# Performance work log

Hardware: AMD Instinct MI355X
Metric: run time of the kernel (lower is better)

## Reference

```python
import jax, jax.numpy as jnp
import numpy as np

B, S, D_IN = 16, 512, 768
HID, OUT = 64, 12
NEG = 1e12


def setup_inputs() -> dict:
    key = jax.random.key(0)
    k1, k2, k3 = jax.random.split(key, 3)
    x = jax.random.normal(k1, (B, S, D_IN), dtype=jnp.float32)
    mask = jnp.ones((B, S), dtype=jnp.float32)
    W = jax.random.normal(k2, (D_IN, HID * OUT * 2), dtype=jnp.float32) * 0.02
    b = jax.random.normal(k3, (HID * OUT * 2,), dtype=jnp.float32) * 0.02
    return {"x": x, "mask": mask, "W": W, "b": b}


def reference(x, mask, W, b):
    Bb, Ss, _ = x.shape
    h, out = HID, OUT
    # QKV-style projection, split into `out` heads of 2h each
    proj = (x @ W + b).reshape(Bb, Ss, out, 2 * h)  # [b, s, out, 2h]
    qw, kw = proj[..., :h], proj[..., h:]           # [b, s, out, h]

    # Sinusoidal position embedding (merge='zero'): interleaved sin/cos
    pos_ids = jnp.arange(Ss, dtype=x.dtype)
    inv_freq = jnp.power(10000.0, -2.0 * jnp.arange(h // 2, dtype=x.dtype) / h)
    ang = pos_ids[:, None] * inv_freq               # [s, h/2]
    sin, cos = jnp.sin(ang), jnp.cos(ang)
    # torch: pos[..., None, 1::2].repeat(1,1,1,2) -> TILED (not interleaved)
    cos_pos = jnp.concatenate([cos, cos], axis=-1)[None, :, None, :]  # [1, s, 1, h]
    sin_pos = jnp.concatenate([sin, sin], axis=-1)[None, :, None, :]

    def rope(w):
        # stack([-w_odd, w_even], -1).reshape -> interleaved rotation partner
        w2 = jnp.stack([-w[..., 1::2], w[..., ::2]], axis=-1).reshape(w.shape)
        return w * cos_pos + w2 * sin_pos

    qw = rope(qw)
    kw = rope(kw)

    logits = jnp.einsum('bmhd,bnhd->bhmn', qw, kw)  # [b, out, s, s]

    pad = mask[:, None, None, :]                    # broadcast over [b, out, s, s]
    logits = logits * pad - (1.0 - pad) * NEG

    tril = jnp.tril(jnp.ones((Ss, Ss), dtype=logits.dtype), -1)
    logits = logits - tril * NEG

    return logits / (h ** 0.5)
```

## Files before the change

### kernel.cpp

```cpp
#include <hip/hip_runtime.h>
#include <stdint.h>

#define DIN   768
#define NPROJ 1536
#define SEQ   512
#define NHEAD 12
#define NBATCH 16
#define NEGV  1000000000000.0f

typedef short bf16x8 __attribute__((ext_vector_type(8)));
typedef float f32x4  __attribute__((ext_vector_type(4)));
typedef unsigned short u16x8 __attribute__((ext_vector_type(8)));

__device__ __forceinline__ unsigned short f2bf(float f) {
    union { float f; unsigned int u; } v; v.f = f;
    return (unsigned short)((v.u + 0x7FFFu + ((v.u >> 16) & 1u)) >> 16);
}
__device__ __forceinline__ float bf2f(unsigned short u) {
    union { unsigned int u; float f; } v; v.u = ((unsigned int)u) << 16;
    return v.f;
}

__device__ __forceinline__ void gl_lds16(const unsigned short* g, unsigned short* l) {
    __builtin_amdgcn_global_load_lds(
        (const __attribute__((address_space(1))) unsigned int*)(uintptr_t)g,
        (__attribute__((address_space(3))) unsigned int*)(uintptr_t)l,
        16, 0, 0);
}

__device__ __forceinline__ void stage128x64(const unsigned short* __restrict__ g,
                                            int gstride, unsigned short* lds,
                                            int w, int lane) {
#pragma unroll
    for (int t = 0; t < 4; t++) {
        int lr = w * 32 + t * 8 + (lane >> 3);
        int c16 = (lane & 7) ^ (lr & 7);
        gl_lds16(g + (size_t)lr * gstride + c16 * 8,
                 lds + (w * 32 + t * 8) * 64);
    }
}
__device__ __forceinline__ int swz(int row, int cg) {
    return row * 64 + ((cg ^ (row & 7)) << 3);
}

__global__ __launch_bounds__(256) void k_prep(const float* __restrict__ X,
                                              unsigned short* __restrict__ Xb,
                                              const float* __restrict__ W,
                                              unsigned short* __restrict__ Wt,
                                              float* __restrict__ trig) {
    __shared__ unsigned short T[64][72];
    const int bid = blockIdx.x, tid = threadIdx.x;
    if (bid < 288) {
        int n0 = (bid % 24) * 64, k0 = (bid / 24) * 64;
#pragma unroll
        for (int it = 0; it < 4; it++) {
            int c = tid + it * 256;
            int kl = c >> 4, nl = (c & 15) * 4;
            float4 v = *(const float4*)&W[(size_t)(k0 + kl) * NPROJ + n0 + nl];
            T[nl + 0][kl] = f2bf(v.x);
            T[nl + 1][kl] = f2bf(v.y);
            T[nl + 2][kl] = f2bf(v.z);
            T[nl + 3][kl] = f2bf(v.w);
        }
        __syncthreads();
#pragma unroll
        for (int it = 0; it < 2; it++) {
            int c = tid + it * 256;
            int nl = c >> 3, kb = (c & 7) * 8;
            *(int4*)&Wt[(size_t)(n0 + nl) * DIN + k0 + kb] = *(int4*)&T[nl][kb];
        }
        return;
    }
    if (bid < 352) {
        int gi = (bid - 288) * 256 + tid;
        int ss = gi >> 5, j = gi & 31;
        const float C = 0.41524101186092034f;
        float cs, sn;
        sincosf((float)ss * exp2f(-(float)j * C), &sn, &cs);
        trig[2 * gi]     = cs;
        trig[2 * gi + 1] = sn;
        return;
    }
    int i = ((bid - 352) * 256 + tid) * 4;
    float4 v = *(const float4*)&X[i];
    short4 s;
    s.x = (short)f2bf(v.x); s.y = (short)f2bf(v.y);
    s.z = (short)f2bf(v.z); s.w = (short)f2bf(v.w);
    *(short4*)&Xb[i] = s;
}

template <bool PRE>
__global__ __launch_bounds__(256) void k_gemm(const float* __restrict__ X,
                                              const unsigned short* __restrict__ Xb,
                                              const unsigned short* __restrict__ Wt,
                                              const float* __restrict__ bias,
                                              const float* __restrict__ trig,
                                              unsigned short* __restrict__ P) {
    __shared__ unsigned short smem[17408];
    unsigned short* sA = smem;
    unsigned short* sB = smem + 8192;
    const int tid = threadIdx.x;
    const int m0 = blockIdx.y * 128, n0 = blockIdx.x * 128;
    const int lane = tid & 63, w = tid >> 6;
    const int q = lane >> 4, r = lane & 15;
    const int wm = w >> 1, wn = w & 1;
    f32x4 acc[4][4];
#pragma unroll
    for (int i = 0; i < 4; i++)
#pragma unroll
        for (int j = 0; j < 4; j++) acc[i][j] = (f32x4){0.f, 0.f, 0.f, 0.f};

    const unsigned short* Ag = Xb + (size_t)m0 * DIN;
    const unsigned short* Bg = Wt + (size_t)n0 * DIN;

    for (int k0 = 0; k0 < DIN; k0 += 64) {
        __syncthreads();
        if (PRE) {
            stage128x64(Ag + k0, DIN, sA, w, lane);
        } else {
#pragma unroll
            for (int it = 0; it < 4; it++) {
                int c = tid + it * 256;
                int row = c >> 3, c16 = c & 7;
                const float* xp = &X[(size_t)(m0 + row) * DIN + k0 + c16 * 8];
                float4 v0 = *(const float4*)xp;
                float4 v1 = *(const float4*)(xp + 4);
                u16x8 sv;
                sv[0] = f2bf(v0.x); sv[1] = f2bf(v0.y);
                sv[2] = f2bf(v0.z); sv[3] = f2bf(v0.w);
                sv[4] = f2bf(v1.x); sv[5] = f2bf(v1.y);
                sv[6] = f2bf(v1.z); sv[7] = f2bf(v1.w);
                *(u16x8*)&sA[swz(row, c16)] = sv;
            }
        }
        stage128x64(Bg + k0, DIN, sB, w, lane);
        __syncthreads();
#pragma unroll
        for (int kk = 0; kk < 64; kk += 32) {
            const int cg = (kk >> 3) + q;
            bf16x8 af[4], bfr[4];
#pragma unroll
            for (int t = 0; t < 4; t++)
                af[t] = *(const bf16x8*)&sA[swz(wm * 64 + t * 16 + r, cg)];
#pragma unroll
            for (int t = 0; t < 4; t++)
                bfr[t] = *(const bf16x8*)&sB[swz(wn * 64 + t * 16 + r, cg)];
#pragma unroll
            for (int tm = 0; tm < 4; tm++)
#pragma unroll
                for (int tn = 0; tn < 4; tn++)
                    acc[tm][tn] = __builtin_amdgcn_mfma_f32_16x16x32_bf16(
                        af[tm], bfr[tn], acc[tm][tn], 0, 0, 0);
        }
    }
    float bb[4];
#pragma unroll
    for (int tn = 0; tn < 4; tn++) bb[tn] = bias[n0 + wn * 64 + tn * 16 + r];
    __syncthreads();
    unsigned short* sT = smem;
#pragma unroll
    for (int tm = 0; tm < 4; tm++) {
        int rowb = wm * 64 + tm * 16 + q * 4;
#pragma unroll
        for (int tn = 0; tn < 4; tn++) {
            int col = wn * 64 + tn * 16 + r;
#pragma unroll
            for (int i = 0; i < 4; i++)
                sT[(rowb + i) * 136 + col] = f2bf(acc[tm][tn][i] + bb[tn]);
        }
    }
    __syncthreads();
#pragma unroll
    for (int it = 0; it < 8; it++) {
        int c = tid + it * 256;
        int row = c >> 4, colb = (c & 15) * 8;
        int m = m0 + row;
        int s = m & (SEQ - 1);
        int base = colb & 31;
        union { int4 v; unsigned short u[8]; } pk;
        pk.v = *(int4*)&sT[row * 136 + colb];
        float wv[8];
#pragma unroll
        for (int j = 0; j < 8; j++) wv[j] = bf2f(pk.u[j]);
        const float* tp = &trig[2 * (s * 32 + base)];
#pragma unroll
        for (int p = 0; p < 4; p++) {
            float4 tt = *(const float4*)&tp[4 * p];
            float oe = wv[2 * p] * tt.x - wv[2 * p + 1] * tt.y;
            float oo = wv[2 * p + 1] * tt.z + wv[2 * p] * tt.w;
            pk.u[2 * p]     = f2bf(oe);
            pk.u[2 * p + 1] = f2bf(oo);
        }
        *(int4*)&P[(size_t)m * NPROJ + n0 + colb] = pk.v;
    }
}

__global__ __launch_bounds__(256) void k_attn(const unsigned short* __restrict__ P,
                                              const float* __restrict__ mask,
                                              float* __restrict__ out) {
    __shared__ unsigned short sQ[8192], sK[8192];
    __shared__ float sbuf[32 * 132];
    const int tid = threadIdx.x;
    const int b = blockIdx.z, h = blockIdx.y, mt = blockIdx.x;
    const int lane = tid & 63, w = tid >> 6;
    const int q = lane >> 4, r = lane & 15;
    const int wm = w >> 1, wn = w & 1;
    const size_t obase = ((size_t)((b * NHEAD + h) * SEQ)) * SEQ;

    const unsigned short* Qg = P + (size_t)(b * SEQ + mt * 128) * NPROJ + h * 128;
    stage128x64(Qg, NPROJ, sQ, w, lane);

    bf16x8 aq[2][4];
    bool qload = false;
    for (int nt = 0; nt < 4; nt++) {
        const int ncol0 = nt * 128;
        if (nt < mt) {
#pragma unroll
            for (int it = 0; it < 16; it++) {
                int c = tid + it * 256;
                int rl = c >> 5, cb = (c & 31) * 4;
                int m = mt * 128 + rl, n = ncol0 + cb;
                f32x4 mk = *(const f32x4*)&mask[b * SEQ + n];
                f32x4 o;
#pragma unroll
                for (int j = 0; j < 4; j++)
                    o[j] = (-(1.f - mk[j]) * NEGV - NEGV) * 0.125f;
                __builtin_nontemporal_store(o, (f32x4*)&out[obase + (size_t)m * SEQ + n]);
            }
            continue;
        }
        __syncthreads();
        const unsigned short* Kg =
            P + (size_t)(b * SEQ + nt * 128) * NPROJ + h * 128 + 64;
        stage128x64(Kg, NPROJ, sK, w, lane);
        __syncthreads();
        if (!qload) {
            qload = true;
#pragma unroll
            for (int x2 = 0; x2 < 2; x2++) {
                int cg = x2 * 4 + q;
#pragma unroll
                for (int t = 0; t < 4; t++)
                    aq[x2][t] = *(const bf16x8*)&sQ[swz(wm * 64 + t * 16 + r, cg)];
            }
        }
        f32x4 acc[4][4];
#pragma unroll
        for (int i = 0; i < 4; i++)
#pragma unroll
            for (int j = 0; j < 4; j++) acc[i][j] = (f32x4){0.f, 0.f, 0.f, 0.f};
#pragma unroll
        for (int x2 = 0; x2 < 2; x2++) {
            int cg = x2 * 4 + q;
            bf16x8 bfr[4];
#pragma unroll
            for (int t = 0; t < 4; t++)
                bfr[t] = *(const bf16x8*)&sK[swz(wn * 64 + t * 16 + r, cg)];
#pragma unroll
            for (int tm = 0; tm < 4; tm++)
#pragma unroll
                for (int tn = 0; tn < 4; tn++)
                    acc[tm][tn] = __builtin_amdgcn_mfma_f32_16x16x32_bf16(
                        aq[x2][tm], bfr[tn], acc[tm][tn], 0, 0, 0);
        }
        const int rowb = wm * 16 + q * 4;
#pragma unroll
        for (int tm = 0; tm < 4; tm++) {
            __syncthreads();
#pragma unroll
            for (int tn = 0; tn < 4; tn++) {
                int col = wn * 64 + tn * 16 + r;
#pragma unroll
                for (int i = 0; i < 4; i++)
                    sbuf[(rowb + i) * 132 + col] = acc[tm][tn][i];
            }
            __syncthreads();
#pragma unroll
            for (int it = 0; it < 4; it++) {
                int c = tid + it * 256;
                int rl = c >> 5, cb = (c & 31) * 4;
                f32x4 v = *(f32x4*)&sbuf[rl * 132 + cb];
                int m = mt * 128 + (rl >> 4) * 64 + tm * 16 + (rl & 15);
                int n = ncol0 + cb;
                f32x4 mk = *(const f32x4*)&mask[b * SEQ + n];
                f32x4 o;
#pragma unroll
                for (int j = 0; j < 4; j++)
                    o[j] = (v[j] * mk[j] - (1.f - mk[j]) * NEGV
                            - ((n + j) < m ? NEGV : 0.f)) * 0.125f;
                __builtin_nontemporal_store(o, (f32x4*)&out[obase + (size_t)m * SEQ + n]);
            }
        }
    }
}

extern "C" void kernel_launch(void* const* d_in, const int* in_sizes, int n_in,
                              void* d_out, int out_size, void* d_ws, size_t ws_size,
                              hipStream_t stream) {
    const float* x    = (const float*)d_in[0];
    const float* mask = (const float*)d_in[1];
    const float* W    = (const float*)d_in[2];
    const float* bias = (const float*)d_in[3];
    float* out = (float*)d_out;

    const size_t wtN   = (size_t)NPROJ * DIN;
    const size_t pN    = (size_t)NBATCH * SEQ * NPROJ;
    const size_t xN    = (size_t)NBATCH * SEQ * DIN;
    const size_t trigN = (size_t)SEQ * 32 * 2;
    unsigned short* Wt = (unsigned short*)d_ws;
    unsigned short* P  = Wt + wtN;
    float* trig        = (float*)(P + pN);
    unsigned short* Xb = (unsigned short*)(trig + trigN);
    const bool pre = ws_size >= (wtN + pN + xN) * sizeof(unsigned short)
                               + trigN * sizeof(float);

    const int xblocks = (int)(xN / 1024);
    k_prep<<<pre ? (352 + xblocks) : 352, 256, 0, stream>>>(x, Xb, W, Wt, trig);
    if (pre) {
        k_gemm<true><<<dim3(NPROJ / 128, (NBATCH * SEQ) / 128), 256, 0, stream>>>(
            x, Xb, Wt, bias, trig, P);
    } else {
        k_gemm<false><<<dim3(NPROJ / 128, (NBATCH * SEQ) / 128), 256, 0, stream>>>(
            x, nullptr, Wt, bias, trig, P);
    }
    k_attn<<<dim3(4, NHEAD, NBATCH), 256, 0, stream>>>(P, mask, out);
}
```

Before: 272.6 us.

## Double-buffer K tiles, store MFMA results directly, remap block order

The attention-logit kernel now double-buffers K tiles in LDS and prefetches the next tile during the current MFMA step. It drops the LDS staging buffer and its per-row-group barriers, writing each accumulator element straight to global memory with scalar nontemporal stores. Block indices are remapped to interleave work across the grid, the fully masked lower tiles are written after the compute loop, and launch bounds request 3 blocks per CU. The cost is narrower, less coalesced 4-byte stores in place of 16-byte vector stores, and Q fragments are reloaded from LDS on every iteration.

```diff
diff --git a/kernel.cpp b/kernel.cpp
--- a/kernel.cpp
+++ b/kernel.cpp
@@ -195,55 +195,34 @@
     }
 }
 
-__global__ __launch_bounds__(256) void k_attn(const unsigned short* __restrict__ P,
-                                              const float* __restrict__ mask,
-                                              float* __restrict__ out) {
-    __shared__ unsigned short sQ[8192], sK[8192];
-    __shared__ float sbuf[32 * 132];
+__global__ __launch_bounds__(256, 3) void k_attn(const unsigned short* __restrict__ P,
+                                                 const float* __restrict__ mask,
+                                                 float* __restrict__ out) {
+    __shared__ unsigned short sQ[8192];
+    __shared__ unsigned short sK[2][8192];
     const int tid = threadIdx.x;
-    const int b = blockIdx.z, h = blockIdx.y, mt = blockIdx.x;
+    int lid = blockIdx.x + 4 * (blockIdx.y + NHEAD * blockIdx.z);
+    lid = (lid & 7) * 96 + (lid >> 3);
+    const int mt = lid & 3;
+    const int h  = (lid >> 2) % NHEAD;
+    const int b  = lid / (4 * NHEAD);
     const int lane = tid & 63, w = tid >> 6;
     const int q = lane >> 4, r = lane & 15;
     const int wm = w >> 1, wn = w & 1;
     const size_t obase = ((size_t)((b * NHEAD + h) * SEQ)) * SEQ;
 
-    const unsigned short* Qg = P + (size_t)(b * SEQ + mt * 128) * NPROJ + h * 128;
-    stage128x64(Qg, NPROJ, sQ, w, lane);
-
-    bf16x8 aq[2][4];
-    bool qload = false;
-    for (int nt = 0; nt < 4; nt++) {
-        const int ncol0 = nt * 128;
-        if (nt < mt) {
-#pragma unroll
-            for (int it = 0; it < 16; it++) {
-                int c = tid + it * 256;
-                int rl = c >> 5, cb = (c & 31) * 4;
-                int m = mt * 128 + rl, n = ncol0 + cb;
-                f32x4 mk = *(const f32x4*)&mask[b * SEQ + n];
-                f32x4 o;
-#pragma unroll
-                for (int j = 0; j < 4; j++)
-                    o[j] = (-(1.f - mk[j]) * NEGV - NEGV) * 0.125f;
-                __builtin_nontemporal_store(o, (f32x4*)&out[obase + (size_t)m * SEQ + n]);
-            }
-            continue;
-        }
+    const unsigned short* Pbh = P + (size_t)b * SEQ * NPROJ + h * 128;
+    stage128x64(Pbh + (size_t)(mt * 128) * NPROJ, NPROJ, sQ, w, lane);
+    stage128x64(Pbh + (size_t)(mt * 128) * NPROJ + 64, NPROJ, sK[0], w, lane);
+
+    int cur = 0;
+    for (int nt = mt; nt < 4; nt++) {
         __syncthreads();
-        const unsigned short* Kg =
-            P + (size_t)(b * SEQ + nt * 128) * NPROJ + h * 128 + 64;
-        stage128x64(Kg, NPROJ, sK, w, lane);
-        __syncthreads();
-        if (!qload) {
-            qload = true;
-#pragma unroll
-            for (int x2 = 0; x2 < 2; x2++) {
-                int cg = x2 * 4 + q;
-#pragma unroll
-                for (int t = 0; t < 4; t++)
-                    aq[x2][t] = *(const bf16x8*)&sQ[swz(wm * 64 + t * 16 + r, cg)];
-            }
-        }
+        if (nt + 1 < 4)
+            stage128x64(Pbh + (size_t)((nt + 1) * 128) * NPROJ + 64, NPROJ,
+                        sK[cur ^ 1], w, lane);
+        const unsigned short* sk = sK[cur];
+
         f32x4 acc[4][4];
 #pragma unroll
         for (int i = 0; i < 4; i++)
@@ -251,45 +230,56 @@
             for (int j = 0; j < 4; j++) acc[i][j] = (f32x4){0.f, 0.f, 0.f, 0.f};
 #pragma unroll
         for (int x2 = 0; x2 < 2; x2++) {
-            int cg = x2 * 4 + q;
-            bf16x8 bfr[4];
+            const int cg = x2 * 4 + q;
+            bf16x8 af[4], bfr[4];
 #pragma unroll
             for (int t = 0; t < 4; t++)
-                bfr[t] = *(const bf16x8*)&sK[swz(wn * 64 + t * 16 + r, cg)];
+                af[t] = *(const bf16x8*)&sQ[swz(wm * 64 + t * 16 + r, cg)];
+#pragma unroll
+            for (int t = 0; t < 4; t++)
+                bfr[t] = *(const bf16x8*)&sk[swz(wn * 64 + t * 16 + r, cg)];
 #pragma unroll
             for (int tm = 0; tm < 4; tm++)
 #pragma unroll
                 for (int tn = 0; tn < 4; tn++)
                     acc[tm][tn] = __builtin_amdgcn_mfma_f32_16x16x32_bf16(
-                        aq[x2][tm], bfr[tn], acc[tm][tn], 0, 0, 0);
-        }
-        const int rowb = wm * 16 + q * 4;
+                        af[tm], bfr[tn], acc[tm][tn], 0, 0, 0);
+        }
+        const int ncol0 = nt * 128;
+        float mkv[4];
+#pragma unroll
+        for (int tn = 0; tn < 4; tn++)
+            mkv[tn] = mask[b * SEQ + ncol0 + wn * 64 + tn * 16 + r];
 #pragma unroll
         for (int tm = 0; tm < 4; tm++) {
-            __syncthreads();
-#pragma unroll
-            for (int tn = 0; tn < 4; tn++) {
-                int col = wn * 64 + tn * 16 + r;
-#pragma unroll
-                for (int i = 0; i < 4; i++)
-                    sbuf[(rowb + i) * 132 + col] = acc[tm][tn][i];
+#pragma unroll
+            for (int i = 0; i < 4; i++) {
+                const int m = mt * 128 + wm * 64 + tm * 16 + q * 4 + i;
+                float* orow = out + obase + (size_t)m * SEQ;
+#pragma unroll
+                for (int tn = 0; tn < 4; tn++) {
+                    const int n = ncol0 + wn * 64 + tn * 16 + r;
+                    float o = (acc[tm][tn][i] * mkv[tn]
+                               - (1.f - mkv[tn]) * NEGV
+                               - (n < m ? NEGV : 0.f)) * 0.125f;
+                    __builtin_nontemporal_store(o, orow + n);
+                }
             }
-            __syncthreads();
-#pragma unroll
-            for (int it = 0; it < 4; it++) {
-                int c = tid + it * 256;
-                int rl = c >> 5, cb = (c & 31) * 4;
-                f32x4 v = *(f32x4*)&sbuf[rl * 132 + cb];
-                int m = mt * 128 + (rl >> 4) * 64 + tm * 16 + (rl & 15);
-                int n = ncol0 + cb;
-                f32x4 mk = *(const f32x4*)&mask[b * SEQ + n];
-                f32x4 o;
-#pragma unroll
-                for (int j = 0; j < 4; j++)
-                    o[j] = (v[j] * mk[j] - (1.f - mk[j]) * NEGV
-                            - ((n + j) < m ? NEGV : 0.f)) * 0.125f;
-                __builtin_nontemporal_store(o, (f32x4*)&out[obase + (size_t)m * SEQ + n]);
-            }
+        }
+        cur ^= 1;
+    }
+    for (int nt = 0; nt < mt; nt++) {
+#pragma unroll
+        for (int it = 0; it < 16; it++) {
+            int c = tid + it * 256;
+            int rl = c >> 5, cb = (c & 31) * 4;
+            int m = mt * 128 + rl, n = nt * 128 + cb;
+            f32x4 mk = *(const f32x4*)&mask[b * SEQ + n];
+            f32x4 o;
+#pragma unroll
+            for (int j = 0; j < 4; j++)
+                o[j] = (-(1.f - mk[j]) * NEGV - NEGV) * 0.125f;
+            __builtin_nontemporal_store(o, (f32x4*)&out[obase + (size_t)m * SEQ + n]);
         }
     }
 }
```

Result: slower. 291.3 us (+6.9%).
